# Kernel optimization log

Measured on AMD Instinct MI355X. Metric: run time of the kernel, lower is better.

## Reference

```python
import jax, jax.numpy as jnp
import numpy as np

ALPHA = 0.2      # LeakyReLU negative slope
NEG = -9e15      # mask fill value from pyGAT dense layer
N, F, H = 4096, 512, 8
NH = F // H      # per-head hidden = 64


def setup_inputs() -> dict:
    key = jax.random.key(0)
    ks = jax.random.split(key, 8)
    x = jax.random.normal(ks[0], (N, F), jnp.float32)
    left = jnp.arange(N, dtype=jnp.int32)  # unused by forward (matches source)
    adj = (jax.random.uniform(ks[1], (N, N)) < 0.01).astype(jnp.float32)
    adj = jnp.minimum(adj + jnp.eye(N, dtype=jnp.float32), 1.0)  # self loops
    Ws = jax.random.normal(ks[2], (H, F, NH), jnp.float32) * (1.0 / np.sqrt(F))
    a1 = jax.random.normal(ks[3], (H, NH), jnp.float32) * 0.1
    a2 = jax.random.normal(ks[4], (H, NH), jnp.float32) * 0.1
    Wo = jax.random.normal(ks[5], (F, F), jnp.float32) * (1.0 / np.sqrt(F))
    ao1 = jax.random.normal(ks[6], (F,), jnp.float32) * 0.1
    ao2 = jax.random.normal(ks[7], (F,), jnp.float32) * 0.1
    return dict(x=x, left=left, adj=adj, Ws=Ws, a1=a1, a2=a2, Wo=Wo, ao1=ao1, ao2=ao2)


def _gat_layer(h, W, a_src, a_dst, adj, concat):
    # h: [N, Fin], W: [Fin, nh]
    Wh = h @ W                                   # [N, nh]
    e = (Wh @ a_src)[:, None] + (Wh @ a_dst)[None, :]   # [N, N]
    e = jnp.where(adj > 0, jax.nn.leaky_relu(e, ALPHA), NEG)
    att = jax.nn.softmax(e, axis=-1)             # row softmax over neighbors
    out = att @ Wh                               # [N, nh]
    return jax.nn.elu(out) if concat else out


def reference(x, left, adj, Ws, a1, a2, Wo, ao1, ao2):
    # multi-head attention (concat=True per head)
    heads = jax.vmap(lambda W, s, d: _gat_layer(x, W, s, d, adj, True))(Ws, a1, a2)  # [H, N, NH]
    hcat = jnp.transpose(heads, (1, 0, 2)).reshape(x.shape[0], H * NH)              # [N, F]
    # output attention layer (concat=False) followed by outer ELU
    out = _gat_layer(hcat, Wo, ao1, ao2, adj, False)
    return jax.nn.elu(out)
```

## Files before the change

kernel.cpp:

```cpp
#include <hip/hip_runtime.h>
#include <hip/hip_bf16.h>
#include <math.h>


#define GN 4096
#define GF 512
#define CAP2 256
#define PS2 260

typedef __attribute__((ext_vector_type(8))) short bf16x8;
typedef __attribute__((ext_vector_type(4))) float f32x4;
typedef __attribute__((ext_vector_type(2))) _Float16 f16x2;
typedef __attribute__((ext_vector_type(4))) _Float16 f16x4;

__device__ inline unsigned short f2bf(float f) {
    unsigned u = __float_as_uint(f);
    return (unsigned short)((u + 0x7fffu + ((u >> 16) & 1u)) >> 16);
}
__device__ inline float bf2f(unsigned short h) {
    return __uint_as_float((unsigned)h << 16);
}
__device__ inline void split2(float v, unsigned short& h, unsigned short& l) {
    h = f2bf(v);
    l = f2bf(v - bf2f(h));
}
__device__ inline void gl16(const void* g, void* l) {
    __builtin_amdgcn_global_load_lds((const __attribute__((address_space(1))) unsigned int*)g,
                                     (__attribute__((address_space(3))) unsigned int*)l, 16, 0, 0);
}

__global__ __launch_bounds__(256) void prep(
        const float* __restrict__ Ws, const float* __restrict__ Wo,
        const float* __restrict__ x,
        unsigned short* __restrict__ wshi, unsigned short* __restrict__ wslo,
        unsigned short* __restrict__ wohi, unsigned short* __restrict__ wolo,
        unsigned short* __restrict__ xhi, unsigned short* __restrict__ xlo) {
    __shared__ float T[64][65];
    int b = blockIdx.x;
    const int t = threadIdx.x;
    if (b < 64) {
        const int h = b >> 3, f0 = (b & 7) * 64;
        #pragma unroll
        for (int i = 0; i < 16; ++i) {
            int idx = i * 256 + t;
            int fr = idx >> 6, k = idx & 63;
            T[fr][k] = Ws[h * 32768 + (f0 + fr) * 64 + k];
        }
        __syncthreads();
        #pragma unroll
        for (int i = 0; i < 16; ++i) {
            int idx = i * 256 + t;
            int k = idx >> 6, fr = idx & 63;
            unsigned short hh, ll;
            split2(T[fr][k], hh, ll);
            size_t dst = (size_t)(h * 64 + k) * 512 + f0 + fr;
            wshi[dst] = hh; wslo[dst] = ll;
        }
        return;
    }
    b -= 64;
    if (b < 64) {
        const int c0 = (b >> 3) * 64, f0 = (b & 7) * 64;
        #pragma unroll
        for (int i = 0; i < 16; ++i) {
            int idx = i * 256 + t;
            int fr = idx >> 6, k = idx & 63;
            T[fr][k] = Wo[(size_t)(f0 + fr) * 512 + c0 + k];
        }
        __syncthreads();
        #pragma unroll
        for (int i = 0; i < 16; ++i) {
            int idx = i * 256 + t;
            int k = idx >> 6, fr = idx & 63;
            unsigned short hh, ll;
            split2(T[fr][k], hh, ll);
            size_t dst = (size_t)(c0 + k) * 512 + f0 + fr;
            wohi[dst] = hh; wolo[dst] = ll;
        }
        return;
    }
    b -= 64;
    {
        int i = b * 256 + t;
        float4 v = ((const float4*)x)[i];
        ushort4 h, l;
        split2(v.x, h.x, l.x); split2(v.y, h.y, l.y);
        split2(v.z, h.z, l.z); split2(v.w, h.w, l.w);
        ((ushort4*)xhi)[i] = h;
        ((ushort4*)xlo)[i] = l;
    }
}

__global__ __launch_bounds__(256) void gemm_3t(
        const unsigned short* __restrict__ Ahi, const unsigned short* __restrict__ Alo,
        const unsigned short* __restrict__ Bhi, const unsigned short* __restrict__ Blo,
        const float* __restrict__ a1v, const float* __restrict__ a2v,
        _Float16* __restrict__ C, float* __restrict__ sdst, float* __restrict__ ddst,
        int M, int K, int Nc) {
    __shared__ char lds[65536];
    const int t = threadIdx.x, lane = t & 63, wid = t >> 6;
    const int blk = blockIdx.x;
    const int bmI = (blk & 7) | ((blk >> 6) << 3);
    const int bnI = (blk >> 3) & 7;
    const int bm0 = bmI * 64, bn0 = bnI * 64;
    const int r0 = t >> 3;
    const int sc8 = (((t & 7) ^ ((t >> 3) & 7)) << 3);
    const size_t aoff = (size_t)(bm0 + r0) * K + sc8;
    const size_t boff = (size_t)(bn0 + r0) * K + sc8;
    const size_t half = (size_t)32 * K;

    auto stage = [&](char* dst, int k0) {
        gl16(Ahi + aoff + k0,        dst + 0 * 4096 + t * 16);
        gl16(Ahi + aoff + half + k0, dst + 1 * 4096 + t * 16);
        gl16(Alo + aoff + k0,        dst + 2 * 4096 + t * 16);
        gl16(Alo + aoff + half + k0, dst + 3 * 4096 + t * 16);
        gl16(Bhi + boff + k0,        dst + 4 * 4096 + t * 16);
        gl16(Bhi + boff + half + k0, dst + 5 * 4096 + t * 16);
        gl16(Blo + boff + k0,        dst + 6 * 4096 + t * 16);
        gl16(Blo + boff + half + k0, dst + 7 * 4096 + t * 16);
    };

    f32x4 acc00 = {0,0,0,0}, acc01 = {0,0,0,0}, acc10 = {0,0,0,0}, acc11 = {0,0,0,0};
    const int mq = (wid >> 1) * 32, nq = (wid & 1) * 32;
    const int rl = lane & 15, hl = lane >> 4;
    const int swz = rl & 7;

    auto compute = [&](const char* Lb) {
        const char* Ah_ = Lb;
        const char* Al_ = Lb + 8192;
        const char* Bh_ = Lb + 16384;
        const char* Bl_ = Lb + 24576;
        #pragma unroll
        for (int s = 0; s < 2; ++s) {
            const int ch = ((s * 4 + hl) ^ swz) * 16;
            const int ra0 = (mq + rl) * 128, ra1 = ra0 + 16 * 128;
            const int rb0 = (nq + rl) * 128, rb1 = rb0 + 16 * 128;
            bf16x8 A0h = *(const bf16x8*)(Ah_ + ra0 + ch);
            bf16x8 A1h = *(const bf16x8*)(Ah_ + ra1 + ch);
            bf16x8 A0l = *(const bf16x8*)(Al_ + ra0 + ch);
            bf16x8 A1l = *(const bf16x8*)(Al_ + ra1 + ch);
            bf16x8 B0h = *(const bf16x8*)(Bh_ + rb0 + ch);
            bf16x8 B1h = *(const bf16x8*)(Bh_ + rb1 + ch);
            bf16x8 B0l = *(const bf16x8*)(Bl_ + rb0 + ch);
            bf16x8 B1l = *(const bf16x8*)(Bl_ + rb1 + ch);
            acc00 = __builtin_amdgcn_mfma_f32_16x16x32_bf16(A0h, B0h, acc00, 0, 0, 0);
            acc01 = __builtin_amdgcn_mfma_f32_16x16x32_bf16(A0h, B1h, acc01, 0, 0, 0);
            acc10 = __builtin_amdgcn_mfma_f32_16x16x32_bf16(A1h, B0h, acc10, 0, 0, 0);
            acc11 = __builtin_amdgcn_mfma_f32_16x16x32_bf16(A1h, B1h, acc11, 0, 0, 0);
            acc00 = __builtin_amdgcn_mfma_f32_16x16x32_bf16(A0h, B0l, acc00, 0, 0, 0);
            acc01 = __builtin_amdgcn_mfma_f32_16x16x32_bf16(A0h, B1l, acc01, 0, 0, 0);
            acc10 = __builtin_amdgcn_mfma_f32_16x16x32_bf16(A1h, B0l, acc10, 0, 0, 0);
            acc11 = __builtin_amdgcn_mfma_f32_16x16x32_bf16(A1h, B1l, acc11, 0, 0, 0);
            acc00 = __builtin_amdgcn_mfma_f32_16x16x32_bf16(A0l, B0h, acc00, 0, 0, 0);
            acc01 = __builtin_amdgcn_mfma_f32_16x16x32_bf16(A0l, B1h, acc01, 0, 0, 0);
            acc10 = __builtin_amdgcn_mfma_f32_16x16x32_bf16(A1l, B0h, acc10, 0, 0, 0);
            acc11 = __builtin_amdgcn_mfma_f32_16x16x32_bf16(A1l, B1h, acc11, 0, 0, 0);
        }
    };

    stage(lds, 0);
    __syncthreads();
    const int NT = K / 64;
    for (int st = 0; st < NT; ++st) {
        char* cur = lds + (st & 1) * 32768;
        if (st + 1 < NT) stage(lds + ((st + 1) & 1) * 32768, (st + 1) * 64);
        compute(cur);
        __syncthreads();
    }

    const int orow = hl * 4;
    #pragma unroll
    for (int j = 0; j < 4; ++j) {
        C[(size_t)(bm0 + mq + orow + j) * Nc + bn0 + nq + rl]           = (_Float16)acc00[j];
        C[(size_t)(bm0 + mq + orow + j) * Nc + bn0 + nq + 16 + rl]      = (_Float16)acc01[j];
        C[(size_t)(bm0 + mq + 16 + orow + j) * Nc + bn0 + nq + rl]      = (_Float16)acc10[j];
        C[(size_t)(bm0 + mq + 16 + orow + j) * Nc + bn0 + nq + 16 + rl] = (_Float16)acc11[j];
    }

    const int C0 = bn0 + nq + rl, C1 = C0 + 16;
    const float a1c0 = a1v[C0], a1c1 = a1v[C1];
    const float a2c0 = a2v[C0], a2c1 = a2v[C1];
    float ps0[4], ps1[4], pd0[4], pd1[4];
    #pragma unroll
    for (int j = 0; j < 4; ++j) {
        ps0[j] = acc00[j] * a1c0 + acc01[j] * a1c1;
        ps1[j] = acc10[j] * a1c0 + acc11[j] * a1c1;
        pd0[j] = acc00[j] * a2c0 + acc01[j] * a2c1;
        pd1[j] = acc10[j] * a2c0 + acc11[j] * a2c1;
    }
    #pragma unroll
    for (int off = 1; off < 16; off <<= 1) {
        #pragma unroll
        for (int j = 0; j < 4; ++j) {
            ps0[j] += __shfl_xor(ps0[j], off);
            ps1[j] += __shfl_xor(ps1[j], off);
            pd0[j] += __shfl_xor(pd0[j], off);
            pd1[j] += __shfl_xor(pd1[j], off);
        }
    }
    float* eps = (float*)lds;
    if ((wid & 1) == 0 && rl == 0) {
        #pragma unroll
        for (int j = 0; j < 4; ++j) {
            eps[mq + orow + j]           = ps0[j];
            eps[mq + 16 + orow + j]      = ps1[j];
            eps[64 + mq + orow + j]      = pd0[j];
            eps[64 + mq + 16 + orow + j] = pd1[j];
        }
    }
    __syncthreads();
    if ((wid & 1) == 1 && rl == 0) {
        #pragma unroll
        for (int j = 0; j < 4; ++j) {
            const int t0 = mq + orow + j, t1 = t0 + 16;
            sdst[(size_t)(bm0 + t0) * 8 + bnI] = ps0[j] + eps[t0];
            sdst[(size_t)(bm0 + t1) * 8 + bnI] = ps1[j] + eps[t1];
            ddst[(size_t)(bm0 + t0) * 8 + bnI] = pd0[j] + eps[64 + t0];
            ddst[(size_t)(bm0 + t1) * 8 + bnI] = pd1[j] + eps[64 + t1];
        }
    }
}

__global__ __launch_bounds__(256) void attn8_kernel(
        const float* __restrict__ adj,
        const _Float16* __restrict__ Wh, const float* __restrict__ s_t,
        const float* __restrict__ d_t,
        unsigned short* __restrict__ nbr, int* __restrict__ deg,
        unsigned short* __restrict__ ohi, unsigned short* __restrict__ olo, int N) {
    __shared__ int nb[2][CAP2];
    __shared__ float p[2][8 * PS2];
    __shared__ float lred[2][8];
    __shared__ int wtot[4];
    const int t = threadIdx.x, lane = t & 63, wv = t >> 6;
    const int rsel = t >> 7, tid = t & 127;
    const int row = blockIdx.x * 2 + rsel;

    const float4* sp = (const float4*)(s_t + (size_t)row * 8);
    const float4 sA = sp[0], sB = sp[1];
    const float shv[8] = {sA.x, sA.y, sA.z, sA.w, sB.x, sB.y, sB.z, sB.w};

    const float4* arow = (const float4*)(adj + (size_t)row * N);
    unsigned m32 = 0;
    #pragma unroll
    for (int q = 0; q < 8; ++q) {
        float4 v = arow[q * 128 + tid];
        if (v.x > 0.f) m32 |= 1u << (q * 4 + 0);
        if (v.y > 0.f) m32 |= 1u << (q * 4 + 1);
        if (v.z > 0.f) m32 |= 1u << (q * 4 + 2);
        if (v.w > 0.f) m32 |= 1u << (q * 4 + 3);
    }
    const int cnt = __popc(m32);
    int inc = cnt;
    #pragma unroll
    for (int off = 1; off < 64; off <<= 1) {
        int nv = __shfl_up(inc, off);
        if (lane >= off) inc += nv;
    }
    if (lane == 63) wtot[wv] = inc;
    __syncthreads();
    const int base = inc - cnt + ((wv & 1) ? wtot[rsel * 2] : 0);
    const int M = wtot[rsel * 2] + wtot[rsel * 2 + 1];
    if (tid == 0) deg[row] = M;
    {
        unsigned m = m32;
        int k = 0;
        while (m) {
            int b = __ffs(m) - 1;
            m &= m - 1;
            int col = ((b >> 2) << 9) + tid * 4 + (b & 3);
            int slot = base + k;
            nb[rsel][slot] = col;
            nbr[(size_t)row * 512 + slot] = (unsigned short)col;
            const float4* dp = (const float4*)(d_t + (size_t)col * 8);
            const float4 dA = dp[0], dB = dp[1];
            const float dv[8] = {dA.x, dA.y, dA.z, dA.w, dB.x, dB.y, dB.z, dB.w};
            #pragma unroll
            for (int h = 0; h < 8; ++h) {
                float e = shv[h] + dv[h];
                e = e > 0.f ? e : 0.2f * e;
                p[rsel][h * PS2 + slot] = e;
            }
            ++k;
        }
    }
    __syncthreads();

    const int h = tid >> 4, sub = tid & 15;
    float lm = -INFINITY;
    for (int j = sub; j < M; j += 16) lm = fmaxf(lm, p[rsel][h * PS2 + j]);
    #pragma unroll
    for (int off = 8; off; off >>= 1) lm = fmaxf(lm, __shfl_xor(lm, off));
    float ls = 0.f;
    for (int j = sub; j < M; j += 16) {
        float pe = __expf(p[rsel][h * PS2 + j] - lm);
        p[rsel][h * PS2 + j] = pe;
        ls += pe;
    }
    #pragma unroll
    for (int off = 8; off; off >>= 1) ls += __shfl_xor(ls, off);
    if (sub == 0) lred[rsel][h] = ls;
    __syncthreads();
    const int c = tid * 4;
    const int hc = tid >> 4;
    const float inv = 1.f / lred[rsel][hc];
    const _Float16* bp = Wh + c;
    const float* prow = &p[rsel][hc * PS2];
    float a0 = 0.f, a1 = 0.f, a2 = 0.f, a3 = 0.f;
    f16x4 w = *(const f16x4*)(bp + (size_t)nb[rsel][0] * 512);
    float pw = prow[0];
    for (int j = 1; j < M; ++j) {
        const f16x4 wn = *(const f16x4*)(bp + (size_t)nb[rsel][j] * 512);
        const float pn = prow[j];
        a0 += pw * (float)w[0]; a1 += pw * (float)w[1];
        a2 += pw * (float)w[2]; a3 += pw * (float)w[3];
        w = wn; pw = pn;
    }
    a0 += pw * (float)w[0]; a1 += pw * (float)w[1];
    a2 += pw * (float)w[2]; a3 += pw * (float)w[3];
    a0 *= inv; a1 *= inv; a2 *= inv; a3 *= inv;
    a0 = a0 > 0.f ? a0 : __expf(a0) - 1.f;
    a1 = a1 > 0.f ? a1 : __expf(a1) - 1.f;
    a2 = a2 > 0.f ? a2 : __expf(a2) - 1.f;
    a3 = a3 > 0.f ? a3 : __expf(a3) - 1.f;
    ushort4 hv, lv;
    split2(a0, hv.x, lv.x); split2(a1, hv.y, lv.y);
    split2(a2, hv.z, lv.z); split2(a3, hv.w, lv.w);
    *(ushort4*)(ohi + (size_t)row * 512 + c) = hv;
    *(ushort4*)(olo + (size_t)row * 512 + c) = lv;
}

__global__ __launch_bounds__(256) void attn1_kernel(
        const _Float16* __restrict__ Wh, const float* __restrict__ s,
        const float* __restrict__ d, const unsigned short* __restrict__ nbr,
        const int* __restrict__ deg, float* __restrict__ out, int N) {
    __shared__ int nb[2][CAP2];
    __shared__ float p[2][CAP2];
    __shared__ float redm[4], reds[4];
    __shared__ float lred[2];
    const int t = threadIdx.x, lane = t & 63, wv = t >> 6;
    const int rsel = t >> 7, tid = t & 127;
    const int row = blockIdx.x * 2 + rsel;
    const int M = deg[row];
    for (int j = tid; j < M; j += 128)
        nb[rsel][j] = nbr[(size_t)row * 512 + j];
    __syncthreads();
    const float4* sp = (const float4*)(s + (size_t)row * 8);
    float4 s0 = sp[0], s1 = sp[1];
    const float sh = ((s0.x + s0.y) + (s0.z + s0.w)) + ((s1.x + s1.y) + (s1.z + s1.w));
    float lm = -INFINITY;
    for (int j = tid; j < M; j += 128) {
        const float4* dp = (const float4*)(d + (size_t)nb[rsel][j] * 8);
        float4 d0 = dp[0], d1 = dp[1];
        float dv = ((d0.x + d0.y) + (d0.z + d0.w)) + ((d1.x + d1.y) + (d1.z + d1.w));
        float e = sh + dv;
        e = e > 0.f ? e : 0.2f * e;
        p[rsel][j] = e;
        lm = fmaxf(lm, e);
    }
    #pragma unroll
    for (int off = 32; off; off >>= 1) lm = fmaxf(lm, __shfl_xor(lm, off));
    if (lane == 0) redm[wv] = lm;
    __syncthreads();
    lm = fmaxf(redm[rsel * 2], redm[rsel * 2 + 1]);
    float ls = 0.f;
    for (int j = tid; j < M; j += 128) {
        float pe = __expf(p[rsel][j] - lm);
        p[rsel][j] = pe;
        ls += pe;
    }
    #pragma unroll
    for (int off = 32; off; off >>= 1) ls += __shfl_xor(ls, off);
    if (lane == 0) reds[wv] = ls;
    __syncthreads();
    if (tid == 0) lred[rsel] = reds[rsel * 2] + reds[rsel * 2 + 1];
    __syncthreads();
    const int c = tid * 4;
    const float inv = 1.f / lred[rsel];
    const _Float16* bp = Wh + c;
    const float* prow = p[rsel];
    float a0 = 0.f, a1 = 0.f, a2 = 0.f, a3 = 0.f;
    f16x4 w = *(const f16x4*)(bp + (size_t)nb[rsel][0] * 512);
    float pw = prow[0];
    for (int j = 1; j < M; ++j) {
        const f16x4 wn = *(const f16x4*)(bp + (size_t)nb[rsel][j] * 512);
        const float pn = prow[j];
        a0 += pw * (float)w[0]; a1 += pw * (float)w[1];
        a2 += pw * (float)w[2]; a3 += pw * (float)w[3];
        w = wn; pw = pn;
    }
    a0 += pw * (float)w[0]; a1 += pw * (float)w[1];
    a2 += pw * (float)w[2]; a3 += pw * (float)w[3];
    a0 *= inv; a1 *= inv; a2 *= inv; a3 *= inv;
    a0 = a0 > 0.f ? a0 : __expf(a0) - 1.f;
    a1 = a1 > 0.f ? a1 : __expf(a1) - 1.f;
    a2 = a2 > 0.f ? a2 : __expf(a2) - 1.f;
    a3 = a3 > 0.f ? a3 : __expf(a3) - 1.f;
    float4 o; o.x = a0; o.y = a1; o.z = a2; o.w = a3;
    *(float4*)(out + (size_t)row * 512 + c) = o;
}

extern "C" void kernel_launch(void* const* d_in, const int* in_sizes, int n_in,
                              void* d_out, int out_size, void* d_ws, size_t ws_size,
                              hipStream_t stream) {
    const float* x   = (const float*)d_in[0];
    const float* adj = (const float*)d_in[2];
    const float* Ws  = (const float*)d_in[3];
    const float* a1  = (const float*)d_in[4];
    const float* a2  = (const float*)d_in[5];
    const float* Wo  = (const float*)d_in[6];
    const float* ao1 = (const float*)d_in[7];
    const float* ao2 = (const float*)d_in[8];
    float* out = (float*)d_out;
    const int N = GN;

    char* wsb = (char*)d_ws;
    _Float16* Whh  = (_Float16*)(wsb + 0);
    _Float16* Whoh = (_Float16*)(wsb + 4194304);
    float* s_t   = (float*)(wsb + 8388608);
    float* d_t   = (float*)(wsb + 8519680);
    float* spart = (float*)(wsb + 8650752);
    float* dpart = (float*)(wsb + 8781824);
    unsigned short* nbrs = (unsigned short*)(wsb + 8912896);
    int*            deg  = (int*)(wsb + 13107200);
    unsigned short* xhi  = (unsigned short*)(wsb + 13123584);
    unsigned short* xlo  = (unsigned short*)(wsb + 17317888);
    unsigned short* hch  = (unsigned short*)(wsb + 21512192);
    unsigned short* hcl  = (unsigned short*)(wsb + 25706496);
    unsigned short* wshi = (unsigned short*)(wsb + 29900800);
    unsigned short* wslo = (unsigned short*)(wsb + 30425088);
    unsigned short* wohi = (unsigned short*)(wsb + 30949376);
    unsigned short* wolo = (unsigned short*)(wsb + 31473664);

    hipLaunchKernelGGL(prep, dim3(2176), dim3(256), 0, stream,
                       Ws, Wo, x, wshi, wslo, wohi, wolo, xhi, xlo);
    hipLaunchKernelGGL(gemm_3t, dim3(512), dim3(256), 0, stream,
                       xhi, xlo, wshi, wslo, a1, a2, Whh, s_t, d_t, 4096, 512, 512);
    hipLaunchKernelGGL(attn8_kernel, dim3(2048), dim3(256), 0, stream,
                       adj, Whh, s_t, d_t, nbrs, deg, hch, hcl, N);
    hipLaunchKernelGGL(gemm_3t, dim3(512), dim3(256), 0, stream,
                       hch, hcl, wohi, wolo, ao1, ao2, Whoh, spart, dpart, 4096, 512, 512);
    hipLaunchKernelGGL(attn1_kernel, dim3(2048), dim3(256), 0, stream,
                       Whoh, spart, dpart, nbrs, deg, out, N);
}
```

Measured before the change: 72.07 us.

## Move adjacency neighbor scan into first GEMM kernel to overlap with compute

The adjacency-row scan that builds the compacted neighbor lists and degrees moves out of the first attention kernel and into the first projection GEMM. Each GEMM block scans 8 rows, odd blocks before their GEMM work and even blocks after it, so the memory-bound scan of the 64MB adjacency can overlap with MFMA work on the same device. The attention kernel then loads the neighbor list from global memory instead of recomputing it. This adds extra barriers and LDS reuse inside the GEMM, lengthens each GEMM block, and adds a global round trip for the neighbor indices.

```diff
diff --git a/kernel.cpp b/kernel.cpp
--- a/kernel.cpp
+++ b/kernel.cpp
@@ -10,7 +10,6 @@
 
 typedef __attribute__((ext_vector_type(8))) short bf16x8;
 typedef __attribute__((ext_vector_type(4))) float f32x4;
-typedef __attribute__((ext_vector_type(2))) _Float16 f16x2;
 typedef __attribute__((ext_vector_type(4))) _Float16 f16x4;
 
 __device__ inline unsigned short f2bf(float f) {
@@ -91,12 +90,14 @@
     }
 }
 
+template<bool SCAN>
 __global__ __launch_bounds__(256) void gemm_3t(
         const unsigned short* __restrict__ Ahi, const unsigned short* __restrict__ Alo,
         const unsigned short* __restrict__ Bhi, const unsigned short* __restrict__ Blo,
         const float* __restrict__ a1v, const float* __restrict__ a2v,
         _Float16* __restrict__ C, float* __restrict__ sdst, float* __restrict__ ddst,
-        int M, int K, int Nc) {
+        const float* __restrict__ adj, unsigned short* __restrict__ nbr,
+        int* __restrict__ deg, int M, int K, int Nc) {
     __shared__ char lds[65536];
     const int t = threadIdx.x, lane = t & 63, wid = t >> 6;
     const int blk = blockIdx.x;
@@ -109,6 +110,53 @@
     const size_t boff = (size_t)(bn0 + r0) * K + sc8;
     const size_t half = (size_t)32 * K;
 
+    auto scan8 = [&]() {
+        int* wt = (int*)lds;
+        #pragma unroll 1
+        for (int r8 = 0; r8 < 8; ++r8) {
+            const int row = blk * 8 + r8;
+            const float4* arow = (const float4*)(adj + (size_t)row * 4096);
+            unsigned m16 = 0;
+            #pragma unroll
+            for (int q = 0; q < 4; ++q) {
+                float4 v = arow[q * 256 + t];
+                if (v.x > 0.f) m16 |= 1u << (q * 4 + 0);
+                if (v.y > 0.f) m16 |= 1u << (q * 4 + 1);
+                if (v.z > 0.f) m16 |= 1u << (q * 4 + 2);
+                if (v.w > 0.f) m16 |= 1u << (q * 4 + 3);
+            }
+            const int cnt = __popc(m16);
+            int inc = cnt;
+            #pragma unroll
+            for (int off = 1; off < 64; off <<= 1) {
+                int nv = __shfl_up(inc, off);
+                if (lane >= off) inc += nv;
+            }
+            if (lane == 63) wt[wid] = inc;
+            __syncthreads();
+            int wb = 0;
+            #pragma unroll
+            for (int w = 0; w < 4; ++w) wb += (w < wid) ? wt[w] : 0;
+            if (t == 0) deg[row] = wt[0] + wt[1] + wt[2] + wt[3];
+            int base = wb + inc - cnt;
+            unsigned m = m16;
+            int k = 0;
+            while (m) {
+                int b = __ffs(m) - 1;
+                m &= m - 1;
+                int col = ((b >> 2) << 10) + t * 4 + (b & 3);
+                nbr[(size_t)row * 512 + base + k] = (unsigned short)col;
+                ++k;
+            }
+            __syncthreads();
+        }
+    };
+
+    f32x4 acc00 = {0,0,0,0}, acc01 = {0,0,0,0}, acc10 = {0,0,0,0}, acc11 = {0,0,0,0};
+    const int mq = (wid >> 1) * 32, nq = (wid & 1) * 32;
+    const int rl = lane & 15, hl = lane >> 4;
+    const int swz = rl & 7;
+
     auto stage = [&](char* dst, int k0) {
         gl16(Ahi + aoff + k0,        dst + 0 * 4096 + t * 16);
         gl16(Ahi + aoff + half + k0, dst + 1 * 4096 + t * 16);
@@ -119,11 +167,6 @@
         gl16(Blo + boff + k0,        dst + 6 * 4096 + t * 16);
         gl16(Blo + boff + half + k0, dst + 7 * 4096 + t * 16);
     };
-
-    f32x4 acc00 = {0,0,0,0}, acc01 = {0,0,0,0}, acc10 = {0,0,0,0}, acc11 = {0,0,0,0};
-    const int mq = (wid >> 1) * 32, nq = (wid & 1) * 32;
-    const int rl = lane & 15, hl = lane >> 4;
-    const int swz = rl & 7;
 
     auto compute = [&](const char* Lb) {
         const char* Ah_ = Lb;
@@ -158,6 +201,11 @@
         }
     };
 
+    if (SCAN && (blk & 1)) {
+        scan8();
+        __syncthreads();
+    }
+
     stage(lds, 0);
     __syncthreads();
     const int NT = K / 64;
@@ -199,6 +247,7 @@
         }
     }
     float* eps = (float*)lds;
+    __syncthreads();
     if ((wid & 1) == 0 && rl == 0) {
         #pragma unroll
         for (int j = 0; j < 4; ++j) {
@@ -219,72 +268,43 @@
             ddst[(size_t)(bm0 + t1) * 8 + bnI] = pd1[j] + eps[64 + t1];
         }
     }
+
+    if (SCAN && !(blk & 1)) {
+        __syncthreads();
+        scan8();
+    }
 }
 
 __global__ __launch_bounds__(256) void attn8_kernel(
-        const float* __restrict__ adj,
         const _Float16* __restrict__ Wh, const float* __restrict__ s_t,
         const float* __restrict__ d_t,
-        unsigned short* __restrict__ nbr, int* __restrict__ deg,
+        const unsigned short* __restrict__ nbr, const int* __restrict__ deg,
         unsigned short* __restrict__ ohi, unsigned short* __restrict__ olo, int N) {
     __shared__ int nb[2][CAP2];
     __shared__ float p[2][8 * PS2];
     __shared__ float lred[2][8];
-    __shared__ int wtot[4];
-    const int t = threadIdx.x, lane = t & 63, wv = t >> 6;
+    const int t = threadIdx.x;
     const int rsel = t >> 7, tid = t & 127;
     const int row = blockIdx.x * 2 + rsel;
-
+    const int M = deg[row];
+    for (int j = tid; j < M; j += 128)
+        nb[rsel][j] = nbr[(size_t)row * 512 + j];
+    __syncthreads();
     const float4* sp = (const float4*)(s_t + (size_t)row * 8);
     const float4 sA = sp[0], sB = sp[1];
     const float shv[8] = {sA.x, sA.y, sA.z, sA.w, sB.x, sB.y, sB.z, sB.w};
-
-    const float4* arow = (const float4*)(adj + (size_t)row * N);
-    unsigned m32 = 0;
-    #pragma unroll
-    for (int q = 0; q < 8; ++q) {
-        float4 v = arow[q * 128 + tid];
-        if (v.x > 0.f) m32 |= 1u << (q * 4 + 0);
-        if (v.y > 0.f) m32 |= 1u << (q * 4 + 1);
-        if (v.z > 0.f) m32 |= 1u << (q * 4 + 2);
-        if (v.w > 0.f) m32 |= 1u << (q * 4 + 3);
-    }
-    const int cnt = __popc(m32);
-    int inc = cnt;
-    #pragma unroll
-    for (int off = 1; off < 64; off <<= 1) {
-        int nv = __shfl_up(inc, off);
-        if (lane >= off) inc += nv;
-    }
-    if (lane == 63) wtot[wv] = inc;
-    __syncthreads();
-    const int base = inc - cnt + ((wv & 1) ? wtot[rsel * 2] : 0);
-    const int M = wtot[rsel * 2] + wtot[rsel * 2 + 1];
-    if (tid == 0) deg[row] = M;
-    {
-        unsigned m = m32;
-        int k = 0;
-        while (m) {
-            int b = __ffs(m) - 1;
-            m &= m - 1;
-            int col = ((b >> 2) << 9) + tid * 4 + (b & 3);
-            int slot = base + k;
-            nb[rsel][slot] = col;
-            nbr[(size_t)row * 512 + slot] = (unsigned short)col;
-            const float4* dp = (const float4*)(d_t + (size_t)col * 8);
-            const float4 dA = dp[0], dB = dp[1];
-            const float dv[8] = {dA.x, dA.y, dA.z, dA.w, dB.x, dB.y, dB.z, dB.w};
-            #pragma unroll
-            for (int h = 0; h < 8; ++h) {
-                float e = shv[h] + dv[h];
-                e = e > 0.f ? e : 0.2f * e;
-                p[rsel][h * PS2 + slot] = e;
-            }
-            ++k;
-        }
-    }
-    __syncthreads();
-
+    for (int j = tid; j < M; j += 128) {
+        const float4* dp = (const float4*)(d_t + (size_t)nb[rsel][j] * 8);
+        const float4 dA = dp[0], dB = dp[1];
+        const float dv[8] = {dA.x, dA.y, dA.z, dA.w, dB.x, dB.y, dB.z, dB.w};
+        #pragma unroll
+        for (int h = 0; h < 8; ++h) {
+            float e = shv[h] + dv[h];
+            e = e > 0.f ? e : 0.2f * e;
+            p[rsel][h * PS2 + j] = e;
+        }
+    }
+    __syncthreads();
     const int h = tid >> 4, sub = tid & 15;
     float lm = -INFINITY;
     for (int j = sub; j < M; j += 16) lm = fmaxf(lm, p[rsel][h * PS2 + j]);
@@ -433,12 +453,15 @@
 
     hipLaunchKernelGGL(prep, dim3(2176), dim3(256), 0, stream,
                        Ws, Wo, x, wshi, wslo, wohi, wolo, xhi, xlo);
-    hipLaunchKernelGGL(gemm_3t, dim3(512), dim3(256), 0, stream,
-                       xhi, xlo, wshi, wslo, a1, a2, Whh, s_t, d_t, 4096, 512, 512);
+    hipLaunchKernelGGL((gemm_3t<true>), dim3(512), dim3(256), 0, stream,
+                       xhi, xlo, wshi, wslo, a1, a2, Whh, s_t, d_t,
+                       adj, nbrs, deg, 4096, 512, 512);
     hipLaunchKernelGGL(attn8_kernel, dim3(2048), dim3(256), 0, stream,
-                       adj, Whh, s_t, d_t, nbrs, deg, hch, hcl, N);
-    hipLaunchKernelGGL(gemm_3t, dim3(512), dim3(256), 0, stream,
-                       hch, hcl, wohi, wolo, ao1, ao2, Whoh, spart, dpart, 4096, 512, 512);
+                       Whh, s_t, d_t, nbrs, deg, hch, hcl, N);
+    hipLaunchKernelGGL((gemm_3t<false>), dim3(512), dim3(256), 0, stream,
+                       hch, hcl, wohi, wolo, ao1, ao2, Whoh, spart, dpart,
+                       (const float*)nullptr, (unsigned short*)nullptr,
+                       (int*)nullptr, 4096, 512, 512);
     hipLaunchKernelGGL(attn1_kernel, dim3(2048), dim3(256), 0, stream,
                        Whoh, spart, dpart, nbrs, deg, out, N);
 }
```

Result: slower. 74.93 us (+4.0%).
